# Performance work log

Hardware: AMD Instinct MI355X
Metric: run time of the kernel (lower is better)

Reference implementation:

```python
import jax, jax.numpy as jnp
import numpy as np

N = 50000       # nodes
E = 500000      # edges (before self-loops)
F_IN = 128      # node feature dim
F_E = 16        # edge feature dim
H = 8           # heads (conv1, conv2)
C1 = 32         # 256 // 8
C2 = 16         # 128 // 8
OUT = 1         # conv3 output channels (1 head, concat=False)
NS = 0.2        # leaky_relu negative slope
EPS = 1e-5      # batchnorm eps


def setup_inputs() -> dict:
    key = jax.random.key(0)
    ks = jax.random.split(key, 32)
    r = lambda k, s: jax.random.normal(k, s, jnp.float32) * 0.1
    inp = {
        'x': jax.random.normal(ks[0], (N, F_IN), jnp.float32),
        'edge_index': jax.random.randint(ks[1], (2, E), 0, N, jnp.int32),
        'edge_attr': jax.random.normal(ks[2], (E, F_E), jnp.float32),
        # conv1 (share_weights=True -> single lin)
        'W1': r(ks[3], (F_IN, H * C1)), 'b1': jnp.zeros((H * C1,), jnp.float32),
        'We1': r(ks[4], (F_E, H * C1)), 'att1': r(ks[5], (H, C1)),
        'bo1': jnp.zeros((H * C1,), jnp.float32),
        'g1': jnp.ones((H * C1,), jnp.float32), 'bt1': jnp.zeros((H * C1,), jnp.float32),
        # conv2 (share_weights=True)
        'W2': r(ks[6], (H * C1, H * C2)), 'b2': jnp.zeros((H * C2,), jnp.float32),
        'We2': r(ks[7], (F_E, H * C2)), 'att2': r(ks[8], (H, C2)),
        'bo2': jnp.zeros((H * C2,), jnp.float32),
        'g2': jnp.ones((H * C2,), jnp.float32), 'bt2': jnp.zeros((H * C2,), jnp.float32),
        # conv3 (share_weights=False -> separate lin_l / lin_r; 1 head, concat=False)
        'W3l': r(ks[9], (H * C2, OUT)), 'b3l': jnp.zeros((OUT,), jnp.float32),
        'W3r': r(ks[10], (H * C2, OUT)), 'b3r': jnp.zeros((OUT,), jnp.float32),
        'We3': r(ks[11], (F_E, OUT)), 'att3': r(ks[12], (1, OUT)),
        'bo3': jnp.zeros((OUT,), jnp.float32),
    }
    return inp


def _gatv2(x, src, dst, eattr, Wl, bl, Wr, br, We, att, bo, heads, ch, concat):
    """One GATv2Conv layer (PyG semantics), edges already include self-loops."""
    n = x.shape[0]
    xl = (x @ Wl + bl).reshape(n, heads, ch)              # source transform
    xr = (x @ Wr + br).reshape(n, heads, ch)              # target transform
    e = (eattr @ We).reshape(-1, heads, ch)               # edge transform (no bias)
    m = xl[src] + xr[dst] + e                             # [Etot, H, C]
    logit = jnp.einsum('ehc,hc->eh', jax.nn.leaky_relu(m, NS), att)
    lmax = jax.ops.segment_max(logit, dst, num_segments=n)
    ex = jnp.exp(logit - lmax[dst])
    denom = jax.ops.segment_sum(ex, dst, num_segments=n)
    alpha = ex / (denom[dst] + 1e-16)                     # segment softmax over dst
    out = jax.ops.segment_sum(alpha[:, :, None] * xl[src], dst, num_segments=n)
    out = out.reshape(n, heads * ch) if concat else out.mean(axis=1)
    return out + bo


def _bn(x, g, b):
    mu = x.mean(axis=0)
    var = ((x - mu) ** 2).mean(axis=0)
    return g * (x - mu) * jax.lax.rsqrt(var + EPS) + b


def reference(x, edge_index, edge_attr, W1, b1, We1, att1, bo1, g1, bt1,
              W2, b2, We2, att2, bo2, g2, bt2,
              W3l, b3l, W3r, b3r, We3, att3, bo3):
    n = x.shape[0]
    # add_self_loops=True with fill_value='mean' for edge_attr (PyG default)
    loop = jnp.arange(n, dtype=edge_index.dtype)
    src = jnp.concatenate([edge_index[0], loop])
    dst = jnp.concatenate([edge_index[1], loop])
    ea = jnp.concatenate([edge_attr,
                          jnp.broadcast_to(edge_attr.mean(axis=0), (n, edge_attr.shape[1]))], axis=0)

    h = _gatv2(x, src, dst, ea, W1, b1, W1, b1, We1, att1, bo1, H, C1, True)
    h = jax.nn.elu(_bn(h, g1, bt1))
    h = _gatv2(h, src, dst, ea, W2, b2, W2, b2, We2, att2, bo2, H, C2, True)
    h = jax.nn.elu(_bn(h, g2, bt2))
    out = _gatv2(h, src, dst, ea, W3l, b3l, W3r, b3r, We3, att3, bo3, 1, OUT, False)
    return out  # [N, 1]
```

## Files before the change

kernel.cpp:

```cpp
#include <hip/hip_runtime.h>

typedef unsigned short u16;
typedef __attribute__((ext_vector_type(4))) float f32x4;
typedef __attribute__((ext_vector_type(2))) float f32x2;
typedef __attribute__((ext_vector_type(8))) short bf16x8;

constexpr int Nn  = 50000;
constexpr int Ee  = 500000;
constexpr int ET  = Nn + Ee;
constexpr int FIN = 128;
constexpr int FE  = 16;
constexpr int Hh  = 8;
constexpr int C1  = 32, HC1 = 256;
constexpr int C2  = 16, HC2 = 128;
constexpr float NS  = 0.2f;
constexpr float EPS = 1e-5f;

__device__ __forceinline__ float b2f(u16 u) { return __uint_as_float(((unsigned)u) << 16); }
__device__ __forceinline__ u16 f2b(float f) {
  unsigned u = __float_as_uint(f);
  u += 0x7FFF + ((u >> 16) & 1);
  return (u16)(u >> 16);
}
__device__ __forceinline__ f32x2 ldbf2(const u16* p) {
  ushort2 u = *reinterpret_cast<const ushort2*>(p);
  return (f32x2){b2f(u.x), b2f(u.y)};
}
__device__ __forceinline__ void stbf2(u16* p, f32x2 v) {
  ushort2 u; u.x = f2b(v.x); u.y = f2b(v.y);
  *reinterpret_cast<ushort2*>(p) = u;
}

template <int RED>
__device__ __forceinline__ float red_sum(float v) {
  v += __int_as_float(__builtin_amdgcn_update_dpp(0, __float_as_int(v), 0xB1, 0xF, 0xF, true));
  v += __int_as_float(__builtin_amdgcn_update_dpp(0, __float_as_int(v), 0x4E, 0xF, 0xF, true));
  v += __int_as_float(__builtin_amdgcn_update_dpp(0, __float_as_int(v), 0x141, 0xF, 0xF, true));
  if constexpr (RED == 16)
    v += __int_as_float(__builtin_amdgcn_update_dpp(0, __float_as_int(v), 0x140, 0xF, 0xF, true));
  return v;
}

__global__ void k_init(int* __restrict__ deg, int* __restrict__ cursor, float* __restrict__ ea_mean,
                       float* __restrict__ bn1s, float* __restrict__ bn1q,
                       float* __restrict__ bn2s, float* __restrict__ bn2q) {
  int t = blockIdx.x * 256 + threadIdx.x;
  int stride = gridDim.x * 256;
  for (int i = t; i < Nn; i += stride) { deg[i] = 0; cursor[i] = 0; }
  if (t < FE) ea_mean[t] = 0.f;
  if (t >= 64 && t < 64 + HC1) { bn1s[t - 64] = 0.f; bn1q[t - 64] = 0.f; }
  if (t >= 384 && t < 384 + HC2) { bn2s[t - 384] = 0.f; bn2q[t - 384] = 0.f; }
}

__global__ void k_deg_mean(const int* __restrict__ ei, const float* __restrict__ ea,
                           int* __restrict__ deg, float* __restrict__ ea_mean) {
  int t = threadIdx.x;
  int e = blockIdx.x * 256 + t;
  if (e < ET) {
    int d = (e < Ee) ? ei[Ee + e] : (e - Ee);
    if ((unsigned)d >= (unsigned)Nn) d = 0;
    atomicAdd(&deg[d], 1);
  }
  __shared__ float s[256];
  int f  = t & 15;
  int r0 = (t >> 4) + blockIdx.x * 16;
  float acc = 0.f;
  for (int r = r0; r < Ee; r += gridDim.x * 16) acc += ea[r * FE + f];
  s[t] = acc;
  __syncthreads();
  if (t < 16) {
    float v = 0.f;
    for (int r = 0; r < 16; r++) v += s[r * 16 + t];
    atomicAdd(&ea_mean[t], v * (1.f / Ee));
  }
}

__global__ __launch_bounds__(1024) void k_scan(const int* __restrict__ deg, int* __restrict__ rowptr) {
  const int T = 1024;
  int t = threadIdx.x;
  const int CH = (Nn + T - 1) / T;
  int base = t * CH;
  int sum = 0;
  for (int i = 0; i < CH; i++) {
    int idx = base + i;
    if (idx < Nn) sum += deg[idx];
  }
  __shared__ int s[T];
  s[t] = sum;
  __syncthreads();
  for (int off = 1; off < T; off <<= 1) {
    int v = (t >= off) ? s[t - off] : 0;
    __syncthreads();
    s[t] += v;
    __syncthreads();
  }
  int run = (t == 0) ? 0 : s[t - 1];
  for (int i = 0; i < CH; i++) {
    int idx = base + i;
    if (idx < Nn) { rowptr[idx] = run; run += deg[idx]; }
  }
  if (t == T - 1) rowptr[Nn] = run;
}

__global__ void k_scatter(const int* __restrict__ ei, const int* __restrict__ rowptr,
                          int* __restrict__ cursor, int2* __restrict__ epack) {
  int e = blockIdx.x * 256 + threadIdx.x;
  if (e >= ET) return;
  int s, d;
  if (e < Ee) { s = ei[e]; d = ei[Ee + e]; } else { s = d = e - Ee; }
  if ((unsigned)s >= (unsigned)Nn) s = 0;
  if ((unsigned)d >= (unsigned)Nn) d = 0;
  int pos = rowptr[d] + atomicAdd(&cursor[d], 1);
  epack[pos] = make_int2(s, e);
}

__global__ void k_bn_coef(const float* __restrict__ sum, const float* __restrict__ sq,
                          const float* __restrict__ g, const float* __restrict__ bt,
                          float2* __restrict__ coef, int HC) {
  int ch = threadIdx.x;
  if (ch >= HC) return;
  float mu = sum[ch] * (1.f / Nn);
  float var = sq[ch] * (1.f / Nn) - mu * mu;
  float rs = rsqrtf(var + EPS);
  float sc = g[ch] * rs;
  coef[ch] = make_float2(sc, bt[ch] - sc * mu);
}

template <int HC>
__global__ void k_bn_stats(const u16* __restrict__ x, float* __restrict__ sum, float* __restrict__ sq) {
  long e0 = (long)blockIdx.x * 256 + threadIdx.x;
  long stride = (long)gridDim.x * 256;
  float s = 0.f, s2 = 0.f;
  for (long e = e0; e < (long)Nn * HC; e += stride) {
    float v = b2f(x[e]);
    s += v; s2 += v * v;
  }
  int ch = (int)(e0 % HC);
  atomicAdd(&sum[ch], s);
  atomicAdd(&sq[ch], s2);
}

template <int KK, int NN, typename AT, bool FUSE>
__global__ __launch_bounds__(256) void k_gemm_mfma(const AT* __restrict__ A, const float* __restrict__ W,
                                                   const float* __restrict__ bias, u16* __restrict__ C,
                                                   const float2* __restrict__ coef, int M) {
  constexpr int WT = KK + 8;
  __shared__ u16 Wt[64 * WT];
  int tid = threadIdx.x;
  int col0 = blockIdx.x * 64;
  int row0 = blockIdx.y * 64;
  for (int idx = tid; idx < KK * 64; idx += 256) {
    int k = idx >> 6, c = idx & 63;
    Wt[c * WT + k] = f2b(W[(size_t)k * NN + col0 + c]);
  }
  __syncthreads();
  int lane = tid & 63;
  int w = tid >> 6;
  int mr = lane & 15, quad = lane >> 4;
  int row = row0 + w * 16 + mr;
  f32x4 acc[4];
#pragma unroll
  for (int t = 0; t < 4; t++) acc[t] = (f32x4){0.f, 0.f, 0.f, 0.f};
  union Frag { bf16x8 v; u16 u[8]; };
  for (int kb = 0; kb < KK; kb += 32) {
    Frag a;
    if (row < M) {
      if constexpr (sizeof(AT) == 4) {
        const float* ap = (const float*)&A[(size_t)row * KK + kb + quad * 8];
        float4 a0 = *reinterpret_cast<const float4*>(ap);
        float4 a1 = *reinterpret_cast<const float4*>(ap + 4);
        a.u[0] = f2b(a0.x); a.u[1] = f2b(a0.y); a.u[2] = f2b(a0.z); a.u[3] = f2b(a0.w);
        a.u[4] = f2b(a1.x); a.u[5] = f2b(a1.y); a.u[6] = f2b(a1.z); a.u[7] = f2b(a1.w);
      } else {
        a.v = *reinterpret_cast<const bf16x8*>(&A[(size_t)row * KK + kb + quad * 8]);
        if constexpr (FUSE) {
          int k0 = kb + quad * 8;
#pragma unroll
          for (int j = 0; j < 8; j++) {
            float2 c2 = coef[k0 + j];
            float y = b2f(a.u[j]) * c2.x + c2.y;
            y = y > 0.f ? y : __expf(y) - 1.f;
            a.u[j] = f2b(y);
          }
        }
      }
    } else {
#pragma unroll
      for (int j = 0; j < 8; j++) a.u[j] = 0;
    }
#pragma unroll
    for (int t = 0; t < 4; t++) {
      const bf16x8* bp = reinterpret_cast<const bf16x8*>(&Wt[(t * 16 + mr) * WT + kb + quad * 8]);
      acc[t] = __builtin_amdgcn_mfma_f32_16x16x32_bf16(a.v, *bp, acc[t], 0, 0, 0);
    }
  }
  int orow = row0 + w * 16 + quad * 4;
#pragma unroll
  for (int t = 0; t < 4; t++) {
    int col = col0 + t * 16 + mr;
    float bs = bias[col];
#pragma unroll
    for (int r = 0; r < 4; r++) {
      int rr = orow + r;
      if (rr < M) C[(size_t)rr * NN + col] = f2b(acc[t][r] + bs);
    }
  }
}

template <int HC, int C, int WPN>
__global__ __launch_bounds__(256) void k_node_attn(
    const int* __restrict__ rowptr, const int2* __restrict__ epack,
    const u16* __restrict__ xl, const float* __restrict__ We, const float* __restrict__ att,
    const float* __restrict__ edge_attr, const float* __restrict__ ea_mean,
    const float* __restrict__ bo, u16* __restrict__ out) {
  int lane = threadIdx.x & 63;
  int gwid = (blockIdx.x << 2) + (threadIdx.x >> 6);
  int nwaves = gridDim.x << 2;
  int w = gwid % WPN;
  int i0 = gwid / WPN;
  int istride = nwaves / WPN;
  int c0 = w * 128 + lane * 2;
  f32x2 w2[FE];
#pragma unroll
  for (int k = 0; k < FE; k++) {
    float2 t = *reinterpret_cast<const float2*>(&We[k * HC + c0]);
    w2[k] = (f32x2){t.x, t.y};
  }
  float at0 = att[c0], at1 = att[c0 + 1];
  f32x2 ews2 = {0.f, 0.f};
#pragma unroll
  for (int k = 0; k < FE; k++) ews2 += ea_mean[k] * w2[k];
  float b0 = bo[c0], b1 = bo[c0 + 1];
  constexpr int RED = C / 2;
  constexpr int UN = 4;

  auto edge_ew = [&](int eid) -> f32x2 {
    if (eid < Ee) {
      const float4* ep = reinterpret_cast<const float4*>(&edge_attr[(size_t)eid * FE]);
      f32x2 a = {0.f, 0.f};
#pragma unroll
      for (int k4 = 0; k4 < 4; k4++) {
        float4 u = ep[k4];
        a += u.x * w2[4 * k4 + 0];
        a += u.y * w2[4 * k4 + 1];
        a += u.z * w2[4 * k4 + 2];
        a += u.w * w2[4 * k4 + 3];
      }
      return a;
    }
    return ews2;
  };

  if (i0 >= Nn) return;
  int p0 = rowptr[i0], p1 = rowptr[i0 + 1];
  ushort2 xdr = *reinterpret_cast<const ushort2*>(&xl[(size_t)i0 * HC + c0]);

  for (int i = i0; i < Nn;) {
    int inext = i + istride;
    int np0 = 0, np1 = 0;
    ushort2 nxdr = make_ushort2(0, 0);
    if (inext < Nn) {
      np0 = rowptr[inext];
      np1 = rowptr[inext + 1];
      nxdr = *reinterpret_cast<const ushort2*>(&xl[(size_t)inext * HC + c0]);
    }
    f32x2 xd = (f32x2){b2f(xdr.x), b2f(xdr.y)};
    int nb = (p1 - p0 + UN - 1) >> 2;
    float m = -1e30f, l = 0.f;
    f32x2 acc = {0.f, 0.f};

    int2 se[UN];
    int pb = p0;
#pragma unroll
    for (int j = 0; j < UN; j++) se[j] = epack[min(pb + j, p1 - 1)];

    for (int b = 0; b < nb; b++) {
      int sA[UN], eA[UN];
#pragma unroll
      for (int j = 0; j < UN; j++) {
        sA[j] = __builtin_amdgcn_readfirstlane(se[j].x);
        eA[j] = __builtin_amdgcn_readfirstlane(se[j].y);
      }
      ushort2 xr[UN];
#pragma unroll
      for (int j = 0; j < UN; j++)
        xr[j] = *reinterpret_cast<const ushort2*>(&xl[(size_t)sA[j] * HC + c0]);
      int pn = pb + UN;
      if (pn < p1) {
#pragma unroll
        for (int j = 0; j < UN; j++) se[j] = epack[min(pn + j, p1 - 1)];
      }
      f32x2 ew[UN];
#pragma unroll
      for (int j = 0; j < UN; j++) ew[j] = edge_ew(eA[j]);
      f32x2 xs[UN];
      float part[UN];
#pragma unroll
      for (int j = 0; j < UN; j++) {
        xs[j] = (f32x2){b2f(xr[j].x), b2f(xr[j].y)};
        f32x2 t = xs[j] + xd + ew[j];
        f32x2 tn = t * NS;
        f32x2 lk = {fmaxf(t.x, tn.x), fmaxf(t.y, tn.y)};
        float pt = lk.x * at0 + lk.y * at1;
        pt = red_sum<RED>(pt);
        part[j] = (pb + j < p1) ? pt : -1e30f;
      }
      float mn = m;
#pragma unroll
      for (int j = 0; j < UN; j++) mn = fmaxf(mn, part[j]);
      float sc = __expf(m - mn);
      float a[UN], asum = 0.f;
      f32x2 ax = {0.f, 0.f};
#pragma unroll
      for (int j = 0; j < UN; j++) {
        a[j] = __expf(part[j] - mn);
        asum += a[j];
        ax += a[j] * xs[j];
      }
      l = l * sc + asum;
      acc = acc * sc + ax;
      m = mn;
      pb = pn;
    }
    float inv = 1.f / (l + 1e-16f);
    f32x2 v = {acc.x * inv + b0, acc.y * inv + b1};
    stbf2(&out[(size_t)i * HC + c0], v);
    i = inext; p0 = np0; p1 = np1; xdr = nxdr;
  }
}

__global__ __launch_bounds__(256) void k_gemv3(const u16* __restrict__ h2,
                                               const float2* __restrict__ coef,
                                               const float* __restrict__ W3l, const float* __restrict__ b3l,
                                               const float* __restrict__ W3r, const float* __restrict__ b3r,
                                               float* __restrict__ xl3, float* __restrict__ xr3) {
  int lane = threadIdx.x & 63;
  int i = (blockIdx.x << 2) + (threadIdx.x >> 6);
  if (i >= Nn) return;
  float2 ca = coef[lane], cb = coef[64 + lane];
  float a = b2f(h2[(long)i * HC2 + lane]) * ca.x + ca.y;
  a = a > 0.f ? a : __expf(a) - 1.f;
  float b = b2f(h2[(long)i * HC2 + 64 + lane]) * cb.x + cb.y;
  b = b > 0.f ? b : __expf(b) - 1.f;
  float pl = a * W3l[lane] + b * W3l[64 + lane];
  float pr = a * W3r[lane] + b * W3r[64 + lane];
  for (int o = 1; o < 64; o <<= 1) { pl += __shfl_xor(pl, o); pr += __shfl_xor(pr, o); }
  if (lane == 0) { xl3[i] = pl + b3l[0]; xr3[i] = pr + b3r[0]; }
}

__global__ __launch_bounds__(256) void k_final3(
    const int* __restrict__ rowptr, const int2* __restrict__ epack,
    const float* __restrict__ xl3, const float* __restrict__ xr3,
    const float* __restrict__ We3, const float* __restrict__ att3,
    const float* __restrict__ edge_attr, const float* __restrict__ ea_mean,
    const float* __restrict__ bo3, float* __restrict__ out) {
  int lane = threadIdx.x & 63;
  int i = (blockIdx.x << 2) + (threadIdx.x >> 6);
  if (i >= Nn) return;
  float we[FE];
#pragma unroll
  for (int k4 = 0; k4 < 4; k4++) {
    float4 u = reinterpret_cast<const float4*>(We3)[k4];
    we[4 * k4] = u.x; we[4 * k4 + 1] = u.y; we[4 * k4 + 2] = u.z; we[4 * k4 + 3] = u.w;
  }
  float at = att3[0];
  float ews = 0.f;
#pragma unroll
  for (int k = 0; k < FE; k++) ews += ea_mean[k] * we[k];
  float xd = xr3[i];
  int p0 = rowptr[i], p1 = rowptr[i + 1];
  float m = -1e30f, l = 0.f, o = 0.f;
  for (int p = p0 + lane; p < p1; p += 64) {
    int2 se = epack[p];
    int s = se.x, eid = se.y;
    float ew;
    if (eid < Ee) {
      const float4* ep = reinterpret_cast<const float4*>(&edge_attr[(size_t)eid * FE]);
      ew = 0.f;
#pragma unroll
      for (int k4 = 0; k4 < 4; k4++) {
        float4 u = ep[k4];
        ew += u.x * we[4 * k4] + u.y * we[4 * k4 + 1] + u.z * we[4 * k4 + 2] + u.w * we[4 * k4 + 3];
      }
    } else ew = ews;
    float xsv = xl3[s];
    float t = xsv + xd + ew;
    float v = t > 0.f ? t : NS * t;
    float logit = v * at;
    float mn = fmaxf(m, logit);
    float sc = __expf(m - mn);
    float a = __expf(logit - mn);
    l = l * sc + a;
    o = o * sc + a * xsv;
    m = mn;
  }
  float M = m;
#pragma unroll
  for (int off = 1; off < 64; off <<= 1) M = fmaxf(M, __shfl_xor(M, off));
  float adj = __expf(m - M);
  float lw = l * adj, ow = o * adj;
#pragma unroll
  for (int off = 1; off < 64; off <<= 1) { lw += __shfl_xor(lw, off); ow += __shfl_xor(ow, off); }
  if (lane == 0) out[i] = ow / (lw + 1e-16f) + bo3[0];
}

extern "C" void kernel_launch(void* const* d_in, const int* in_sizes, int n_in,
                              void* d_out, int out_size, void* d_ws, size_t ws_size,
                              hipStream_t stream) {
  const float* x    = (const float*)d_in[0];
  const int*   ei   = (const int*)d_in[1];
  const float* ea   = (const float*)d_in[2];
  const float* W1   = (const float*)d_in[3];
  const float* b1   = (const float*)d_in[4];
  const float* We1  = (const float*)d_in[5];
  const float* att1 = (const float*)d_in[6];
  const float* bo1  = (const float*)d_in[7];
  const float* g1   = (const float*)d_in[8];
  const float* bt1  = (const float*)d_in[9];
  const float* W2   = (const float*)d_in[10];
  const float* b2   = (const float*)d_in[11];
  const float* We2  = (const float*)d_in[12];
  const float* att2 = (const float*)d_in[13];
  const float* bo2  = (const float*)d_in[14];
  const float* g2   = (const float*)d_in[15];
  const float* bt2  = (const float*)d_in[16];
  const float* W3l  = (const float*)d_in[17];
  const float* b3l  = (const float*)d_in[18];
  const float* W3r  = (const float*)d_in[19];
  const float* b3r  = (const float*)d_in[20];
  const float* We3  = (const float*)d_in[21];
  const float* att3 = (const float*)d_in[22];
  const float* bo3  = (const float*)d_in[23];
  float* out = (float*)d_out;

  char* ws = (char*)d_ws;
  size_t off = 0;
  auto alloc = [&](size_t bytes) -> void* {
    void* p = ws + off;
    off = (off + bytes + 255) & ~(size_t)255;
    return p;
  };
  int*    deg     = (int*)alloc((size_t)Nn * 4);
  int*    rowptr  = (int*)alloc((size_t)(Nn + 1) * 4);
  int*    cursor  = (int*)alloc((size_t)Nn * 4);
  int2*   epack   = (int2*)alloc((size_t)ET * 8);
  float*  ea_mean = (float*)alloc((size_t)FE * 4);
  float*  bn1s    = (float*)alloc(256 * 4);
  float*  bn1q    = (float*)alloc(256 * 4);
  float*  bn2s    = (float*)alloc(128 * 4);
  float*  bn2q    = (float*)alloc(128 * 4);
  float2* bncoef  = (float2*)alloc(256 * 8);
  float*  xl3     = (float*)alloc((size_t)Nn * 4);
  float*  xr3     = (float*)alloc((size_t)Nn * 4);
  u16*    xlA     = (u16*)alloc((size_t)Nn * 256 * 2);
  u16*    hB      = (u16*)alloc((size_t)Nn * 256 * 2);

  k_init<<<512, 256, 0, stream>>>(deg, cursor, ea_mean, bn1s, bn1q, bn2s, bn2q);
  k_deg_mean<<<(ET + 255) / 256, 256, 0, stream>>>(ei, ea, deg, ea_mean);
  k_scan<<<1, 1024, 0, stream>>>(deg, rowptr);
  k_scatter<<<(ET + 255) / 256, 256, 0, stream>>>(ei, rowptr, cursor, epack);

  k_gemm_mfma<FIN, HC1, float, false><<<dim3(HC1 / 64, (Nn + 63) / 64), 256, 0, stream>>>(
      x, W1, b1, xlA, nullptr, Nn);
  k_node_attn<HC1, C1, 2><<<2048, 256, 0, stream>>>(rowptr, epack, xlA, We1, att1,
                                                    ea, ea_mean, bo1, hB);
  k_bn_stats<HC1><<<256, 256, 0, stream>>>(hB, bn1s, bn1q);
  k_bn_coef<<<1, 256, 0, stream>>>(bn1s, bn1q, g1, bt1, bncoef, HC1);

  k_gemm_mfma<HC1, HC2, u16, true><<<dim3(HC2 / 64, (Nn + 63) / 64), 256, 0, stream>>>(
      hB, W2, b2, xlA, bncoef, Nn);
  k_node_attn<HC2, C2, 1><<<2048, 256, 0, stream>>>(rowptr, epack, xlA, We2, att2,
                                                    ea, ea_mean, bo2, hB);
  k_bn_stats<HC2><<<256, 256, 0, stream>>>(hB, bn2s, bn2q);
  k_bn_coef<<<1, 256, 0, stream>>>(bn2s, bn2q, g2, bt2, bncoef, HC2);

  k_gemv3<<<(Nn + 3) / 4, 256, 0, stream>>>(hB, bncoef, W3l, b3l, W3r, b3r, xl3, xr3);
  k_final3<<<(Nn + 3) / 4, 256, 0, stream>>>(rowptr, epack, xl3, xr3, We3, att3,
                                             ea, ea_mean, bo3, out);
}
```

Baseline: 729.0 us.

## Software-pipeline gathers and edge-attr loads one block ahead in node attention

Restructures the per-node edge loop in k_node_attn so that the next block's source-feature gathers and edge_attr rows are issued before the current block's softmax math runs. The edge_attr dot product is computed from registers on the following iteration. The goal is to hide global gather latency behind compute. It also folds log2(e) into the attention vector so the code can call exp2 directly instead of __expf. The cost is higher register pressure from the prefetched rows (4 float4 per edge times UN), which may lower occupancy.

```diff
diff --git a/kernel.cpp b/kernel.cpp
--- a/kernel.cpp
+++ b/kernel.cpp
@@ -15,6 +15,7 @@
 constexpr int C2  = 16, HC2 = 128;
 constexpr float NS  = 0.2f;
 constexpr float EPS = 1e-5f;
+constexpr float LOG2E = 1.44269504088896340736f;
 
 __device__ __forceinline__ float b2f(u16 u) { return __uint_as_float(((unsigned)u) << 16); }
 __device__ __forceinline__ u16 f2b(float f) {
@@ -226,7 +227,7 @@
     float2 t = *reinterpret_cast<const float2*>(&We[k * HC + c0]);
     w2[k] = (f32x2){t.x, t.y};
   }
-  float at0 = att[c0], at1 = att[c0 + 1];
+  float at0 = att[c0] * LOG2E, at1 = att[c0 + 1] * LOG2E;
   f32x2 ews2 = {0.f, 0.f};
 #pragma unroll
   for (int k = 0; k < FE; k++) ews2 += ea_mean[k] * w2[k];
@@ -234,21 +235,25 @@
   constexpr int RED = C / 2;
   constexpr int UN = 4;
 
-  auto edge_ew = [&](int eid) -> f32x2 {
-    if (eid < Ee) {
-      const float4* ep = reinterpret_cast<const float4*>(&edge_attr[(size_t)eid * FE]);
-      f32x2 a = {0.f, 0.f};
-#pragma unroll
-      for (int k4 = 0; k4 < 4; k4++) {
-        float4 u = ep[k4];
-        a += u.x * w2[4 * k4 + 0];
-        a += u.y * w2[4 * k4 + 1];
-        a += u.z * w2[4 * k4 + 2];
-        a += u.w * w2[4 * k4 + 3];
-      }
-      return a;
-    }
-    return ews2;
+  struct EaRow { float4 r[4]; };
+  auto ea_issue = [&](int eid) -> EaRow {
+    int ec = (eid < Ee) ? eid : 0;
+    const float4* ep = reinterpret_cast<const float4*>(&edge_attr[(size_t)ec * FE]);
+    EaRow e;
+    e.r[0] = ep[0]; e.r[1] = ep[1]; e.r[2] = ep[2]; e.r[3] = ep[3];
+    return e;
+  };
+  auto ea_dot = [&](int eid, const EaRow& e) -> f32x2 {
+    f32x2 a = {0.f, 0.f};
+#pragma unroll
+    for (int k4 = 0; k4 < 4; k4++) {
+      float4 u = e.r[k4];
+      a += u.x * w2[4 * k4 + 0];
+      a += u.y * w2[4 * k4 + 1];
+      a += u.z * w2[4 * k4 + 2];
+      a += u.w * w2[4 * k4 + 3];
+    }
+    return (eid < Ee) ? a : ews2;
   };
 
   if (i0 >= Nn) return;
@@ -269,58 +274,78 @@
     float m = -1e30f, l = 0.f;
     f32x2 acc = {0.f, 0.f};
 
-    int2 se[UN];
-    int pb = p0;
-#pragma unroll
-    for (int j = 0; j < UN; j++) se[j] = epack[min(pb + j, p1 - 1)];
-
+    int2 seN[UN];
+#pragma unroll
+    for (int j = 0; j < UN; j++) seN[j] = epack[min(p0 + j, p1 - 1)];
+    ushort2 xrC[UN];
+    EaRow  erC[UN];
+    int    eidC[UN];
+#pragma unroll
+    for (int j = 0; j < UN; j++) {
+      int s = __builtin_amdgcn_readfirstlane(seN[j].x);
+      eidC[j] = __builtin_amdgcn_readfirstlane(seN[j].y);
+      xrC[j] = *reinterpret_cast<const ushort2*>(&xl[(size_t)s * HC + c0]);
+      erC[j] = ea_issue(eidC[j]);
+    }
+#pragma unroll
+    for (int j = 0; j < UN; j++) seN[j] = epack[min(p0 + UN + j, p1 - 1)];
+    f32x2 ewC[UN];
+#pragma unroll
+    for (int j = 0; j < UN; j++) ewC[j] = ea_dot(eidC[j], erC[j]);
+
+    int pc = p0;
     for (int b = 0; b < nb; b++) {
-      int sA[UN], eA[UN];
-#pragma unroll
-      for (int j = 0; j < UN; j++) {
-        sA[j] = __builtin_amdgcn_readfirstlane(se[j].x);
-        eA[j] = __builtin_amdgcn_readfirstlane(se[j].y);
+      int pn = pc + UN;
+      bool more = pn < p1;
+      ushort2 xrN[UN];
+      EaRow  erN[UN];
+      int    eidN[UN];
+      if (more) {
+#pragma unroll
+        for (int j = 0; j < UN; j++) {
+          int s = __builtin_amdgcn_readfirstlane(seN[j].x);
+          eidN[j] = __builtin_amdgcn_readfirstlane(seN[j].y);
+          xrN[j] = *reinterpret_cast<const ushort2*>(&xl[(size_t)s * HC + c0]);
+          erN[j] = ea_issue(eidN[j]);
+        }
+#pragma unroll
+        for (int j = 0; j < UN; j++) seN[j] = epack[min(pn + UN + j, p1 - 1)];
       }
-      ushort2 xr[UN];
-#pragma unroll
-      for (int j = 0; j < UN; j++)
-        xr[j] = *reinterpret_cast<const ushort2*>(&xl[(size_t)sA[j] * HC + c0]);
-      int pn = pb + UN;
-      if (pn < p1) {
-#pragma unroll
-        for (int j = 0; j < UN; j++) se[j] = epack[min(pn + j, p1 - 1)];
-      }
-      f32x2 ew[UN];
-#pragma unroll
-      for (int j = 0; j < UN; j++) ew[j] = edge_ew(eA[j]);
       f32x2 xs[UN];
       float part[UN];
 #pragma unroll
       for (int j = 0; j < UN; j++) {
-        xs[j] = (f32x2){b2f(xr[j].x), b2f(xr[j].y)};
-        f32x2 t = xs[j] + xd + ew[j];
+        xs[j] = (f32x2){b2f(xrC[j].x), b2f(xrC[j].y)};
+        f32x2 t = xs[j] + xd + ewC[j];
         f32x2 tn = t * NS;
         f32x2 lk = {fmaxf(t.x, tn.x), fmaxf(t.y, tn.y)};
         float pt = lk.x * at0 + lk.y * at1;
         pt = red_sum<RED>(pt);
-        part[j] = (pb + j < p1) ? pt : -1e30f;
+        part[j] = (pc + j < p1) ? pt : -1e30f;
       }
       float mn = m;
 #pragma unroll
       for (int j = 0; j < UN; j++) mn = fmaxf(mn, part[j]);
-      float sc = __expf(m - mn);
+      float sc = __builtin_amdgcn_exp2f(m - mn);
       float a[UN], asum = 0.f;
       f32x2 ax = {0.f, 0.f};
 #pragma unroll
       for (int j = 0; j < UN; j++) {
-        a[j] = __expf(part[j] - mn);
+        a[j] = __builtin_amdgcn_exp2f(part[j] - mn);
         asum += a[j];
         ax += a[j] * xs[j];
       }
       l = l * sc + asum;
       acc = acc * sc + ax;
       m = mn;
-      pb = pn;
+      if (more) {
+#pragma unroll
+        for (int j = 0; j < UN; j++) {
+          ewC[j] = ea_dot(eidN[j], erN[j]);
+          xrC[j] = xrN[j];
+        }
+      }
+      pc = pn;
     }
     float inv = 1.f / (l + 1e-16f);
     f32x2 v = {acc.x * inv + b0, acc.y * inv + b1};
```

After: 819.6 us. +12.4%, slower.

## Split GATv2 attention into edge-parallel logit pass and node-wise softmax combine

Applied to the files above, without the earlier changes.

Replaces the fused per-node attention kernel for conv1 and conv2 with two kernels. The first computes per-edge, per-head logits in even edge-range chunks, which balances load across waves regardless of node degree, and stores them to workspace. The second does an online softmax per node using exp2 on logits prescaled by log2(e), unrolled four edges at a time, and aggregates the source features. This trades an extra workspace round trip of ET*8 logits and a second gather of source features for better load balance and less dependent latency. The old fused kernel remains as a fallback when the workspace is too small.

```diff
diff --git a/kernel.cpp b/kernel.cpp
--- a/kernel.cpp
+++ b/kernel.cpp
@@ -15,6 +15,7 @@
 constexpr int C2  = 16, HC2 = 128;
 constexpr float NS  = 0.2f;
 constexpr float EPS = 1e-5f;
+constexpr float LOG2E = 1.44269504088896340736f;
 
 __device__ __forceinline__ float b2f(u16 u) { return __uint_as_float(((unsigned)u) << 16); }
 __device__ __forceinline__ u16 f2b(float f) {
@@ -204,6 +205,168 @@
       int rr = orow + r;
       if (rr < M) C[(size_t)rr * NN + col] = f2b(acc[t][r] + bs);
     }
+  }
+}
+
+template <int HC, int C, int WPN, typename LT>
+__global__ __launch_bounds__(256) void k_edge_logit(
+    const int* __restrict__ rowptr, const int2* __restrict__ epack,
+    const u16* __restrict__ xl, const float* __restrict__ We,
+    const float* __restrict__ att, const float* __restrict__ edge_attr,
+    const float* __restrict__ ea_mean, LT* __restrict__ logit) {
+  int lane = threadIdx.x & 63;
+  int gwid = (blockIdx.x << 2) + (threadIdx.x >> 6);
+  int nw = gridDim.x << 2;
+  int w = gwid % WPN;
+  int eg = gwid / WPN;
+  int ng = nw / WPN;
+  int chunk = (ET + ng - 1) / ng;
+  int pbeg = eg * chunk;
+  int pend = min(pbeg + chunk, ET);
+  if (pbeg >= pend) return;
+  int c0 = w * 128 + lane * 2;
+  f32x2 w2[FE];
+#pragma unroll
+  for (int k = 0; k < FE; k++) {
+    float2 t = *reinterpret_cast<const float2*>(&We[k * HC + c0]);
+    w2[k] = (f32x2){t.x, t.y};
+  }
+  float at0 = att[c0] * LOG2E, at1 = att[c0 + 1] * LOG2E;
+  f32x2 ews2 = {0.f, 0.f};
+#pragma unroll
+  for (int k = 0; k < FE; k++) ews2 += ea_mean[k] * w2[k];
+  constexpr int RED = C / 2;
+  int hd = c0 / C;
+  bool writer = (lane & (RED - 1)) == 0;
+
+  int lo = 0, hi = Nn - 1;
+  while (lo < hi) {
+    int mid = (lo + hi + 1) >> 1;
+    if (rowptr[mid] <= pbeg) lo = mid; else hi = mid - 1;
+  }
+  int node = lo;
+  int p1i = rowptr[node + 1];
+  ushort2 xdr = *reinterpret_cast<const ushort2*>(&xl[(size_t)node * HC + c0]);
+
+  int2 se0 = epack[pbeg];
+  int sC = __builtin_amdgcn_readfirstlane(se0.x);
+  int eidC = __builtin_amdgcn_readfirstlane(se0.y);
+  const float4* epc = reinterpret_cast<const float4*>(
+      &edge_attr[(size_t)((eidC < Ee) ? eidC : 0) * FE]);
+  float4 ea0 = epc[0], ea1 = epc[1], ea2 = epc[2], ea3 = epc[3];
+
+  for (int p = pbeg; p < pend; ++p) {
+    while (p >= p1i) {
+      ++node;
+      p1i = rowptr[node + 1];
+      xdr = *reinterpret_cast<const ushort2*>(&xl[(size_t)node * HC + c0]);
+    }
+    int s = sC, eid = eidC;
+    float4 c0_ = ea0, c1_ = ea1, c2_ = ea2, c3_ = ea3;
+    ushort2 xsr = *reinterpret_cast<const ushort2*>(&xl[(size_t)s * HC + c0]);
+    if (p + 1 < pend) {
+      int2 seN = epack[p + 1];
+      sC = __builtin_amdgcn_readfirstlane(seN.x);
+      eidC = __builtin_amdgcn_readfirstlane(seN.y);
+      const float4* epn = reinterpret_cast<const float4*>(
+          &edge_attr[(size_t)((eidC < Ee) ? eidC : 0) * FE]);
+      ea0 = epn[0]; ea1 = epn[1]; ea2 = epn[2]; ea3 = epn[3];
+    }
+    f32x2 ew;
+    if (eid < Ee) {
+      f32x2 a = {0.f, 0.f};
+      a += c0_.x * w2[0];  a += c0_.y * w2[1];  a += c0_.z * w2[2];  a += c0_.w * w2[3];
+      a += c1_.x * w2[4];  a += c1_.y * w2[5];  a += c1_.z * w2[6];  a += c1_.w * w2[7];
+      a += c2_.x * w2[8];  a += c2_.y * w2[9];  a += c2_.z * w2[10]; a += c2_.w * w2[11];
+      a += c3_.x * w2[12]; a += c3_.y * w2[13]; a += c3_.z * w2[14]; a += c3_.w * w2[15];
+      ew = a;
+    } else {
+      ew = ews2;
+    }
+    f32x2 xs = (f32x2){b2f(xsr.x), b2f(xsr.y)};
+    f32x2 xd = (f32x2){b2f(xdr.x), b2f(xdr.y)};
+    f32x2 t = xs + xd + ew;
+    f32x2 tn = t * NS;
+    f32x2 lk = {fmaxf(t.x, tn.x), fmaxf(t.y, tn.y)};
+    float pt = lk.x * at0 + lk.y * at1;
+    pt = red_sum<RED>(pt);
+    if (writer) logit[(size_t)p * Hh + hd] = (LT)pt;
+  }
+}
+
+template <int HC, int C, int WPN, typename LT>
+__global__ __launch_bounds__(256) void k_node_combine(
+    const int* __restrict__ rowptr, const int2* __restrict__ epack,
+    const u16* __restrict__ xl, const LT* __restrict__ logit,
+    const float* __restrict__ bo, u16* __restrict__ out) {
+  int lane = threadIdx.x & 63;
+  int gwid = (blockIdx.x << 2) + (threadIdx.x >> 6);
+  int nwaves = gridDim.x << 2;
+  int w = gwid % WPN;
+  int i0 = gwid / WPN;
+  int istride = nwaves / WPN;
+  int c0 = w * 128 + lane * 2;
+  int hd = c0 / C;
+  float b0 = bo[c0], b1 = bo[c0 + 1];
+  constexpr int UN = 4;
+
+  for (int i = i0; i < Nn; i += istride) {
+    int p0 = rowptr[i], p1 = rowptr[i + 1];
+    float m = -1e30f, l = 0.f;
+    f32x2 acc = {0.f, 0.f};
+    int nb = (p1 - p0 + UN - 1) >> 2;
+
+    int2 se[UN];
+    float lg[UN];
+#pragma unroll
+    for (int j = 0; j < UN; j++) {
+      int pc = min(p0 + j, p1 - 1);
+      se[j] = epack[pc];
+      lg[j] = (float)logit[(size_t)pc * Hh + hd];
+    }
+
+    int pb = p0;
+    for (int b = 0; b < nb; b++) {
+      int sA[UN];
+#pragma unroll
+      for (int j = 0; j < UN; j++) sA[j] = __builtin_amdgcn_readfirstlane(se[j].x);
+      ushort2 xr[UN];
+#pragma unroll
+      for (int j = 0; j < UN; j++)
+        xr[j] = *reinterpret_cast<const ushort2*>(&xl[(size_t)sA[j] * HC + c0]);
+      float part[UN];
+#pragma unroll
+      for (int j = 0; j < UN; j++) part[j] = (pb + j < p1) ? lg[j] : -1e30f;
+      int pn = pb + UN;
+      if (pn < p1) {
+#pragma unroll
+        for (int j = 0; j < UN; j++) {
+          int pc = min(pn + j, p1 - 1);
+          se[j] = epack[pc];
+          lg[j] = (float)logit[(size_t)pc * Hh + hd];
+        }
+      }
+      float mn = m;
+#pragma unroll
+      for (int j = 0; j < UN; j++) mn = fmaxf(mn, part[j]);
+      float sc = __builtin_amdgcn_exp2f(m - mn);
+      float a[UN], asum = 0.f;
+      f32x2 ax = {0.f, 0.f};
+#pragma unroll
+      for (int j = 0; j < UN; j++) {
+        a[j] = __builtin_amdgcn_exp2f(part[j] - mn);
+        f32x2 xs = (f32x2){b2f(xr[j].x), b2f(xr[j].y)};
+        asum += a[j];
+        ax += a[j] * xs;
+      }
+      l = l * sc + asum;
+      acc = acc * sc + ax;
+      m = mn;
+      pb = pn;
+    }
+    float inv = 1.f / (l + 1e-16f);
+    f32x2 v = {acc.x * inv + b0, acc.y * inv + b1};
+    stbf2(&out[(size_t)i * HC + c0], v);
   }
 }
 
@@ -454,6 +617,10 @@
   float*  xr3     = (float*)alloc((size_t)Nn * 4);
   u16*    xlA     = (u16*)alloc((size_t)Nn * 256 * 2);
   u16*    hB      = (u16*)alloc((size_t)Nn * 256 * 2);
+  size_t off_common = off;
+  void*  logit_raw = (void*)(ws + off_common);
+  size_t need_f32 = off_common + (size_t)ET * Hh * 4;
+  size_t need_f16 = off_common + (size_t)ET * Hh * 2;
 
   k_init<<<512, 256, 0, stream>>>(deg, cursor, ea_mean, bn1s, bn1q, bn2s, bn2q);
   k_deg_mean<<<(ET + 255) / 256, 256, 0, stream>>>(ei, ea, deg, ea_mean);
@@ -462,15 +629,40 @@
 
   k_gemm_mfma<FIN, HC1, float, false><<<dim3(HC1 / 64, (Nn + 63) / 64), 256, 0, stream>>>(
       x, W1, b1, xlA, nullptr, Nn);
-  k_node_attn<HC1, C1, 2><<<2048, 256, 0, stream>>>(rowptr, epack, xlA, We1, att1,
-                                                    ea, ea_mean, bo1, hB);
+
+  if (ws_size >= need_f32) {
+    float* logit = (float*)logit_raw;
+    k_edge_logit<HC1, C1, 2, float><<<2048, 256, 0, stream>>>(rowptr, epack, xlA, We1, att1,
+                                                              ea, ea_mean, logit);
+    k_node_combine<HC1, C1, 2, float><<<2048, 256, 0, stream>>>(rowptr, epack, xlA, logit, bo1, hB);
+  } else if (ws_size >= need_f16) {
+    _Float16* logit = (_Float16*)logit_raw;
+    k_edge_logit<HC1, C1, 2, _Float16><<<2048, 256, 0, stream>>>(rowptr, epack, xlA, We1, att1,
+                                                                 ea, ea_mean, logit);
+    k_node_combine<HC1, C1, 2, _Float16><<<2048, 256, 0, stream>>>(rowptr, epack, xlA, logit, bo1, hB);
+  } else {
+    k_node_attn<HC1, C1, 2><<<2048, 256, 0, stream>>>(rowptr, epack, xlA, We1, att1,
+                                                      ea, ea_mean, bo1, hB);
+  }
   k_bn_stats<HC1><<<256, 256, 0, stream>>>(hB, bn1s, bn1q);
   k_bn_coef<<<1, 256, 0, stream>>>(bn1s, bn1q, g1, bt1, bncoef, HC1);
 
   k_gemm_mfma<HC1, HC2, u16, true><<<dim3(HC2 / 64, (Nn + 63) / 64), 256, 0, stream>>>(
       hB, W2, b2, xlA, bncoef, Nn);
-  k_node_attn<HC2, C2, 1><<<2048, 256, 0, stream>>>(rowptr, epack, xlA, We2, att2,
-                                                    ea, ea_mean, bo2, hB);
+  if (ws_size >= need_f32) {
+    float* logit = (float*)logit_raw;
+    k_edge_logit<HC2, C2, 1, float><<<2048, 256, 0, stream>>>(rowptr, epack, xlA, We2, att2,
+                                                              ea, ea_mean, logit);
+    k_node_combine<HC2, C2, 1, float><<<2048, 256, 0, stream>>>(rowptr, epack, xlA, logit, bo2, hB);
+  } else if (ws_size >= need_f16) {
+    _Float16* logit = (_Float16*)logit_raw;
+    k_edge_logit<HC2, C2, 1, _Float16><<<2048, 256, 0, stream>>>(rowptr, epack, xlA, We2, att2,
+                                                                 ea, ea_mean, logit);
+    k_node_combine<HC2, C2, 1, _Float16><<<2048, 256, 0, stream>>>(rowptr, epack, xlA, logit, bo2, hB);
+  } else {
+    k_node_attn<HC2, C2, 1><<<2048, 256, 0, stream>>>(rowptr, epack, xlA, We2, att2,
+                                                      ea, ea_mean, bo2, hB);
+  }
   k_bn_stats<HC2><<<256, 256, 0, stream>>>(hB, bn2s, bn2q);
   k_bn_coef<<<1, 256, 0, stream>>>(bn2s, bn2q, g2, bt2, bncoef, HC2);
 
```

New measurement: 945.4 us. 29.7% more time.
